# Performance work log

Measured on AMD Instinct MI355X. Metric: run time of the kernel, lower is better.

Reference implementation:

```python
import jax, jax.numpy as jnp
import numpy as np

NUM_CLASSES = 80
PRE_NMS_K = 400    # pre_nms_points / max_output_size_per_class
MAX_BOXES = 200    # max_total_size
NMS_THRESH = 0.6
SCORE_THRESH = 0.0  # iou_thresh in YoloLayer, used as score threshold/mask
SCALE_XY = (1.2, 1.1, 1.05)  # levels 3,4,5
STRIDES = (8.0, 16.0, 32.0)  # 2**level


def setup_inputs() -> dict:
    key = jax.random.key(0)
    k3, k4, k5 = jax.random.split(key, 3)
    B, C5 = 8, 3 * (NUM_CLASSES + 5)
    p3 = jax.random.normal(k3, (B, 64, 64, C5), dtype=jnp.float32)
    p4 = jax.random.normal(k4, (B, 32, 32, C5), dtype=jnp.float32)
    p5 = jax.random.normal(k5, (B, 16, 16, C5), dtype=jnp.float32)
    a3 = jnp.array([[12., 16.], [19., 36.], [40., 28.]], jnp.float32)
    a4 = jnp.array([[36., 75.], [76., 55.], [72., 146.]], jnp.float32)
    a5 = jnp.array([[142., 110.], [192., 243.], [459., 401.]], jnp.float32)
    return {"p3": p3, "p4": p4, "p5": p5, "a3": a3, "a4": a4, "a5": a5}


def _decode_level(p, anchors, stride, scale_xy):
    # p: [B,H,W,A*(C+5)] raw head output; 'original' box decode (sigmoid xy, exp wh)
    B, H, W, _ = p.shape
    A = anchors.shape[0]
    d = p.reshape(B, H, W, A, NUM_CLASSES + 5)
    txy, twh, tobj, tcls = d[..., :2], d[..., 2:4], d[..., 4:5], d[..., 5:]
    gx, gy = jnp.meshgrid(jnp.arange(W, dtype=p.dtype), jnp.arange(H, dtype=p.dtype))
    grid = jnp.stack([gx, gy], -1)[None, :, :, None, :]          # [1,H,W,1,2] (x,y)
    sxy = jnp.asarray(scale_xy, p.dtype)
    xy = (jax.nn.sigmoid(txy) * sxy - 0.5 * (sxy - 1.0) + grid) / jnp.array([W, H], p.dtype)
    wh = jnp.exp(twh) * anchors[None, None, None] / jnp.array([W * stride, H * stride], p.dtype)
    x1y1 = xy - 0.5 * wh
    x2y2 = xy + 0.5 * wh
    boxes = jnp.stack([x1y1[..., 1], x1y1[..., 0], x2y2[..., 1], x2y2[..., 0]], -1)  # yxyx
    obj = jax.nn.sigmoid(tobj)
    cls = jax.nn.sigmoid(tcls) * obj
    N = H * W * A
    return boxes.reshape(B, N, 4), cls.reshape(B, N, NUM_CLASSES), obj.reshape(B, N)


def _pairwise_iou(b):
    # b: [K,4] yxyx in [0,1]
    area = (b[:, 2] - b[:, 0]) * (b[:, 3] - b[:, 1])
    tl = jnp.maximum(b[:, None, :2], b[None, :, :2])
    br = jnp.minimum(b[:, None, 2:], b[None, :, 2:])
    wh = jnp.maximum(br - tl, 0.0)
    inter = wh[..., 0] * wh[..., 1]
    union = area[:, None] + area[None, :] - inter
    return inter / jnp.maximum(union, 1e-9)


def _greedy_nms_scores(boxes, scores):
    # boxes/scores already sorted by score descending; returns scores with suppressed -> 0
    K = scores.shape[0]
    overlap = _pairwise_iou(boxes) > NMS_THRESH
    idx = jnp.arange(K)

    def body(i, keep):
        sup = overlap[i] & (idx > i) & keep[i]
        return keep & ~sup

    keep = jax.lax.fori_loop(0, K, body, jnp.ones((K,), bool))
    return jnp.where(keep & (scores > SCORE_THRESH), scores, 0.0)


def _detections_per_image(boxes, cls_scores):
    # boxes [N,4], cls_scores [N,C] -> combined per-class NMS, top MAX_BOXES overall
    boxes = jnp.clip(boxes, 0.0, 1.0)  # combined NMS clips boxes by default

    def per_class(scores_c):
        vals, idx = jax.lax.top_k(scores_c, PRE_NMS_K)
        b = boxes[idx]
        return _greedy_nms_scores(b, vals), b

    kept_scores, kept_boxes = jax.vmap(per_class)(cls_scores.T)  # [C,K], [C,K,4]
    flat_s = kept_scores.reshape(-1)
    flat_b = kept_boxes.reshape(-1, 4)
    cls_ids = jnp.repeat(jnp.arange(NUM_CLASSES), PRE_NMS_K)
    top_s, top_i = jax.lax.top_k(flat_s, MAX_BOXES)
    top_b = flat_b[top_i]
    top_c = cls_ids[top_i].astype(jnp.float32)
    valid = top_s > 0.0
    top_b = jnp.where(valid[:, None], top_b, 0.0)
    top_c = jnp.where(valid, top_c, 0.0)
    num = jnp.sum(valid.astype(jnp.int32))
    return top_b, top_s, top_c, num


def _forward(p3, p4, p5, a3, a4, a5):
    boxes, cls_scores, obj_scores = [], [], []
    for (p, a), stride, sxy in zip(((p3, a3), (p4, a4), (p5, a5)), STRIDES, SCALE_XY):
        b, c, o = _decode_level(p, a, stride, sxy)
        boxes.append(b); cls_scores.append(c); obj_scores.append(o)
    boxes = jnp.concatenate(boxes, 1)            # [B,N,4]
    cls_scores = jnp.concatenate(cls_scores, 1)  # [B,N,C]
    obj_scores = jnp.concatenate(obj_scores, 1)  # [B,N]
    obj_mask = (obj_scores > SCORE_THRESH).astype(boxes.dtype)
    cls_mask = (cls_scores > SCORE_THRESH).astype(boxes.dtype)
    cls_scores = cls_scores * obj_mask[..., None] * cls_mask
    return jax.vmap(_detections_per_image)(boxes, cls_scores)


def reference(p3, p4, p5, a3, a4, a5):
    bbox, confidence, classes, num_detections = _forward(p3, p4, p5, a3, a4, a5)
    return bbox, confidence, classes, num_detections
```

## Files before the change

kernel.cpp:

```cpp
#include <hip/hip_runtime.h>
#include <math.h>

#define NCLS 80
#define PRE_K 400
#define MAX_BOXES 200
#define KEEP_CAP 200
#define N_TOT 16128
#define M_FIN (NCLS * KEEP_CAP)
#define NMS_T 0.6f
#define NTHR 512
#define CAP 512

typedef unsigned long long u64;
typedef unsigned int u32;

__device__ __forceinline__ float sigf(float x) { return 1.0f / (1.0f + expf(-x)); }

__device__ __forceinline__ void hist_agg(u32* hist, u32 d, bool valid, int lane)
{
    u64 act = __ballot(valid);
    while (act) {
        int ldr = __ffsll((unsigned long long)act) - 1;
        u32 dl = __shfl(d, ldr, 64);
        u64 m = __ballot(valid && d == dl);
        if (lane == ldr) atomicAdd(&hist[dl], (u32)__popcll(m));
        act &= ~m;
    }
}

__device__ __forceinline__ void digit_select(const u32* hist, int need,
                                             u32* sh_dg, u32* sh_S1, u32* sh_T, int tid)
{
    if (tid < 64) {
        const int lane = tid;
        u32 h0 = hist[4 * lane + 0], h1 = hist[4 * lane + 1];
        u32 h2 = hist[4 * lane + 2], h3 = hist[4 * lane + 3];
        u32 loc = h0 + h1 + h2 + h3;
        u32 s = loc;
#pragma unroll
        for (int off = 1; off < 64; off <<= 1) {
            u32 t = __shfl_down(s, off, 64);
            if (lane + off < 64) s += t;
        }
        u32 after = s - loc;
        u32 S3 = h3 + after, S2 = h2 + S3, S1v = h1 + S2, S0 = h0 + S1v;
        u32 Sarr[5] = { S0, S1v, S2, S3, after };
#pragma unroll
        for (int k = 0; k < 4; ++k) {
            if ((int)Sarr[k] >= need && need > (int)Sarr[k + 1]) {
                *sh_dg = (u32)(4 * lane + k);
                *sh_S1 = Sarr[k + 1];
                *sh_T  = Sarr[k] - Sarr[k + 1];
            }
        }
    }
    __syncthreads();
}

__device__ __forceinline__ void radix_topk_sort(
    const u32* __restrict__ keys, int n, int K,
    u64* cand, u32* hist, u32* scr,
    u32* sh_dg, u32* sh_S1, u32* sh_T, int* sh_gcnt, int tid)
{
    int need = K;
    digit_select(hist, need, sh_dg, sh_S1, sh_T, tid);
    u32 thr = *sh_dg; need -= (int)*sh_S1;
    int C = (K - need) + (int)*sh_T;
    int eshift = 24;

    const uint4* k4 = (const uint4*)keys;
    const int n4 = n >> 2;
    const int nIter = (n4 + NTHR - 1) / NTHR;

    for (int shift = 16; shift >= 0 && C > CAP; shift -= 8) {
        if (tid < 256) hist[tid] = 0u;
        __syncthreads();
        for (int it = 0; it < nIter; ++it) {
            int i4 = tid + it * NTHR;
            if (i4 < n4) {
                uint4 kk = k4[i4];
                if ((kk.x >> (shift + 8)) == thr) atomicAdd(&hist[(kk.x >> shift) & 255u], 1u);
                if ((kk.y >> (shift + 8)) == thr) atomicAdd(&hist[(kk.y >> shift) & 255u], 1u);
                if ((kk.z >> (shift + 8)) == thr) atomicAdd(&hist[(kk.z >> shift) & 255u], 1u);
                if ((kk.w >> (shift + 8)) == thr) atomicAdd(&hist[(kk.w >> shift) & 255u], 1u);
            }
        }
        __syncthreads();
        digit_select(hist, need, sh_dg, sh_S1, sh_T, tid);
        thr = (thr << 8) | *sh_dg; need -= (int)*sh_S1;
        C = (K - need) + (int)*sh_T;
        eshift = shift;
    }

    if (C <= CAP) {
        for (int it = 0; it < nIter; ++it) {
            int i4 = tid + it * NTHR;
            if (i4 < n4) {
                uint4 kk = k4[i4];
                int i0 = i4 << 2;
                if ((kk.x >> eshift) >= thr) { int p = atomicAdd(sh_gcnt, 1); cand[p] = ((u64)kk.x << 32) | (u32)(0xFFFFFFFFu - (u32)(i0 + 0)); }
                if ((kk.y >> eshift) >= thr) { int p = atomicAdd(sh_gcnt, 1); cand[p] = ((u64)kk.y << 32) | (u32)(0xFFFFFFFFu - (u32)(i0 + 1)); }
                if ((kk.z >> eshift) >= thr) { int p = atomicAdd(sh_gcnt, 1); cand[p] = ((u64)kk.z << 32) | (u32)(0xFFFFFFFFu - (u32)(i0 + 2)); }
                if ((kk.w >> eshift) >= thr) { int p = atomicAdd(sh_gcnt, 1); cand[p] = ((u64)kk.w << 32) | (u32)(0xFFFFFFFFu - (u32)(i0 + 3)); }
            }
        }
        __syncthreads();
        for (int t = C + tid; t < CAP; t += NTHR) cand[t] = 0ull;
    } else {
        for (int i = tid; i < n; i += NTHR) {
            u32 k = keys[i];
            if (k > thr) {
                int p = atomicAdd(sh_gcnt, 1);
                cand[p] = ((u64)k << 32) | (u32)(0xFFFFFFFFu - (u32)i);
            }
        }
        __syncthreads();
        const int G = *sh_gcnt;
        int lo = tid * 32; if (lo > n) lo = n;
        int hi = lo + 32;  if (hi > n) hi = n;
        int lc = 0;
        for (int i = lo; i < hi; ++i) if (keys[i] == thr) ++lc;
        u32* sc_cur = scr; u32* sc_oth = scr + 512;
        sc_cur[tid] = (u32)lc;
        __syncthreads();
        for (int off = 1; off < NTHR; off <<= 1) {
            sc_oth[tid] = sc_cur[tid] + ((tid >= off) ? sc_cur[tid - off] : 0u);
            __syncthreads();
            u32* tmp = sc_cur; sc_cur = sc_oth; sc_oth = tmp;
        }
        int r = (int)sc_cur[tid] - lc;
        for (int i = lo; i < hi; ++i) {
            if (keys[i] == thr) {
                if (r < need) cand[G + r] = ((u64)thr << 32) | (u32)(0xFFFFFFFFu - (u32)i);
                ++r;
            }
        }
        __syncthreads();
        for (int t = K + tid; t < CAP; t += NTHR) cand[t] = 0ull;
    }
    __syncthreads();

    u64 v = cand[tid];
#pragma unroll
    for (int k2 = 2; k2 <= 64; k2 <<= 1) {
#pragma unroll
        for (int j = k2 >> 1; j > 0; j >>= 1) {
            u64 p = __shfl_xor(v, j, 64);
            bool takeMax = ((tid & k2) == 0) ^ ((tid & j) != 0);
            v = takeMax ? (v >= p ? v : p) : (v <= p ? v : p);
        }
    }
    for (int k2 = 128; k2 <= CAP; k2 <<= 1) {
        for (int j = k2 >> 1; j >= 64; j >>= 1) {
            __syncthreads();
            cand[tid] = v;
            __syncthreads();
            u64 p = cand[tid ^ j];
            bool takeMax = ((tid & k2) == 0) ^ ((tid & j) != 0);
            v = takeMax ? (v >= p ? v : p) : (v <= p ? v : p);
        }
#pragma unroll
        for (int j = 32; j > 0; j >>= 1) {
            u64 p = __shfl_xor(v, j, 64);
            bool takeMax = ((tid & k2) == 0) ^ ((tid & j) != 0);
            v = takeMax ? (v >= p ? v : p) : (v <= p ? v : p);
        }
    }
    __syncthreads();
    cand[tid] = v;
    __syncthreads();
}

__global__ __launch_bounds__(256) void decode_kernel(
    const float* __restrict__ p3, const float* __restrict__ p4, const float* __restrict__ p5,
    const float* __restrict__ a3, const float* __restrict__ a4, const float* __restrict__ a5,
    float* __restrict__ scores, float* __restrict__ boxes)
{
    const int blk = blockIdx.x;
    const int b = blk & 7;
    const int n = ((blk >> 3) << 8) + threadIdx.x;

    const float* base; const float* anc; int logw, nn; float sx;
    if (n < 12288)      { base = p3; anc = a3; logw = 6; nn = n;         sx = 1.2f;  }
    else if (n < 15360) { base = p4; anc = a4; logw = 5; nn = n - 12288; sx = 1.1f;  }
    else                { base = p5; anc = a5; logw = 4; nn = n - 15360; sx = 1.05f; }
    const int W = 1 << logw;
    const int a = nn % 3; const int hw = nn / 3;
    const int w = hw & (W - 1); const int h = hw >> logw;
    const float winv = 1.0f / (float)W;
    const float* rec = base + ((size_t)((b * W + h) * W + w) * 255 + a * 85);

    float tx = rec[0], ty = rec[1], tw = rec[2], th = rec[3], to = rec[4];
    float sobj = sigf(to);
    float cx = (sigf(tx) * sx - 0.5f * (sx - 1.0f) + (float)w) * winv;
    float cy = (sigf(ty) * sx - 0.5f * (sx - 1.0f) + (float)h) * winv;
    float bw = expf(tw) * anc[a * 2 + 0] * (1.0f / 512.0f);
    float bh = expf(th) * anc[a * 2 + 1] * (1.0f / 512.0f);
    float x1 = cx - 0.5f * bw, x2 = cx + 0.5f * bw;
    float y1 = cy - 0.5f * bh, y2 = cy + 0.5f * bh;
    y1 = fminf(fmaxf(y1, 0.f), 1.f); x1 = fminf(fmaxf(x1, 0.f), 1.f);
    y2 = fminf(fmaxf(y2, 0.f), 1.f); x2 = fminf(fmaxf(x2, 0.f), 1.f);
    float4 bb; bb.x = y1; bb.y = x1; bb.z = y2; bb.w = x2;
    ((float4*)boxes)[b * N_TOT + n] = bb;

    float* sb = scores + (long)b * NCLS * N_TOT + n;
#pragma unroll 8
    for (int cc = 0; cc < NCLS; ++cc)
        sb[(long)cc * N_TOT] = sigf(rec[5 + cc]) * sobj;
}

__global__ __launch_bounds__(NTHR, 8) void topk_nms_fused(
    const float* __restrict__ scores, const float* __restrict__ boxes,
    float* __restrict__ ksc, float* __restrict__ kbox)
{
    __shared__ alignas(16) u64 cand[CAP];
    __shared__ u32 hist[260];
    __shared__ u32 sh_dg, sh_S1, sh_T;
    __shared__ int sh_gcnt;
    __shared__ alignas(16) u64 sup[PRE_K * 7];
    __shared__ float by1[448], bx1[448], by2[448], bx2[448], bar[448];
    __shared__ u64 keepw[7];
    __shared__ int wpre[8];
    __shared__ int sh_ncnt;

    const int tid = threadIdx.x;
    const int wv = tid >> 6;
    const int lane = tid & 63;
    const int b = blockIdx.x & 7;
    const int c = blockIdx.x >> 3;

    const u32* keys = (const u32*)(scores + (long)(b * NCLS + c) * N_TOT);

    if (tid < 260) hist[tid] = 0u;
    if (tid == 0) sh_gcnt = 0;
    __syncthreads();
    const uint4* k4 = (const uint4*)keys;
#pragma unroll
    for (int it = 0; it < 8; ++it) {
        int i4 = tid + it * NTHR;
        bool v = i4 < (N_TOT >> 2);
        u32 d0 = 0, d1 = 0, d2 = 0, d3 = 0;
        if (v) {
            uint4 kk = k4[i4];
            d0 = kk.x >> 24; d1 = kk.y >> 24; d2 = kk.z >> 24; d3 = kk.w >> 24;
        }
        hist_agg(hist, d0, v, lane);
        hist_agg(hist, d1, v, lane);
        hist_agg(hist, d2, v, lane);
        hist_agg(hist, d3, v, lane);
    }
    __syncthreads();

    radix_topk_sort(keys, N_TOT, PRE_K, cand, hist, (u32*)sup,
                    &sh_dg, &sh_S1, &sh_T, &sh_gcnt, tid);

    for (int t = tid; t < PRE_K * 7; t += NTHR) sup[t] = 0ull;

    const float4* btab = (const float4*)boxes;
    for (int t = tid; t < 448; t += NTHR) {
        float y1 = 0.f, x1 = 0.f, y2 = 0.f, x2 = 0.f;
        if (t < PRE_K) {
            u64 key = cand[t];
            if ((key >> 32) != 0ull) {
                int idx = (int)(0xFFFFFFFFu - (u32)(key & 0xFFFFFFFFull));
                float4 bb = btab[b * N_TOT + idx];
                y1 = bb.x; x1 = bb.y; y2 = bb.z; x2 = bb.w;
            }
        }
        by1[t] = y1; bx1[t] = x1; by2[t] = y2; bx2[t] = x2;
        bar[t] = (y2 - y1) * (x2 - x1);
    }
    __syncthreads();

    for (int row = wv; row < PRE_K; row += 8) {
        float ry1 = by1[row], rx1 = bx1[row], ry2 = by2[row], rx2 = bx2[row], ra = bar[row];
        int c0 = (row + 1) >> 6;
        for (int cw = c0; cw < 7; ++cw) {
            int j = (cw << 6) + lane;
            bool o = false;
            if (j > row && j < PRE_K) {
                float ty = fmaxf(ry1, by1[j]);
                float tx = fmaxf(rx1, bx1[j]);
                float by = fminf(ry2, by2[j]);
                float rx = fminf(rx2, bx2[j]);
                float hh = fmaxf(by - ty, 0.f);
                float ww = fmaxf(rx - tx, 0.f);
                float inter = hh * ww;
                float uni = ra + bar[j] - inter;
                o = (inter / fmaxf(uni, 1e-9f)) > NMS_T;
            }
            u64 m = __ballot(o);
            if (lane == 0) sup[row * 7 + cw] = m;
        }
    }
    __syncthreads();

    if (tid < 64) {
        u64 kw = (tid < 6) ? ~0ull : ((tid == 6) ? 0xFFFFull : 0ull);
        u64 s_cur = (tid < 7) ? sup[tid] : 0ull;
        for (int i = 0; i < PRE_K; ++i) {
            u64 s_next = (tid < 7 && (i + 1) < PRE_K) ? sup[(i + 1) * 7 + tid] : 0ull;
            u64 kwv = __shfl(kw, i >> 6);
            if ((kwv >> (i & 63)) & 1ull) kw &= ~s_cur;
            s_cur = s_next;
        }
        if (tid < 7) keepw[tid] = kw;
    }
    __syncthreads();

    if (tid == 0) {
        int acc = 0;
        for (int w = 0; w < 7; ++w) { wpre[w] = acc; acc += (int)__popcll(keepw[w]); }
        sh_ncnt = acc < KEEP_CAP ? acc : KEEP_CAP;
    }
    __syncthreads();

    const int blk_out = b * NCLS + c;
    float* osc = ksc + (long)blk_out * KEEP_CAP;
    float* obx = kbox + (long)blk_out * KEEP_CAP * 4;
    for (int t = tid; t < PRE_K; t += NTHR) {
        int w = t >> 6, bb = t & 63;
        u64 kwv = keepw[w];
        if ((kwv >> bb) & 1ull) {
            int pos = wpre[w] + (int)__popcll(kwv & ((1ull << bb) - 1ull));
            if (pos < KEEP_CAP) {
                osc[pos] = __uint_as_float((u32)(cand[t] >> 32));
                obx[pos * 4 + 0] = by1[t]; obx[pos * 4 + 1] = bx1[t];
                obx[pos * 4 + 2] = by2[t]; obx[pos * 4 + 3] = bx2[t];
            }
        }
    }
    for (int t = sh_ncnt + tid; t < KEEP_CAP; t += NTHR) {
        osc[t] = 0.0f;
        obx[t * 4 + 0] = 0.f; obx[t * 4 + 1] = 0.f;
        obx[t * 4 + 2] = 0.f; obx[t * 4 + 3] = 0.f;
    }
}

__global__ __launch_bounds__(NTHR, 4) void topk_nms_mono(
    const float* __restrict__ p3, const float* __restrict__ p4, const float* __restrict__ p5,
    const float* __restrict__ a3, const float* __restrict__ a4, const float* __restrict__ a5,
    float* __restrict__ ksc, float* __restrict__ kbox)
{
    __shared__ alignas(16) u32 skey[N_TOT];
    __shared__ alignas(16) u64 cand[CAP];
    __shared__ u32 hist[260];
    __shared__ u32 scr[1024];
    __shared__ u32 sh_dg, sh_S1, sh_T;
    __shared__ int sh_gcnt;
    __shared__ u64 keepw[7];
    __shared__ int wpre[8];
    __shared__ int sh_ncnt;

    const int tid = threadIdx.x;
    const int wv = tid >> 6;
    const int lane = tid & 63;
    const int b = blockIdx.x & 7;
    const int c = blockIdx.x >> 3;

    if (tid < 260) hist[tid] = 0u;
    if (tid == 0) sh_gcnt = 0;
    __syncthreads();
    for (int i = tid; i < N_TOT; i += NTHR) {
        const float* base; int H, W, n;
        if (i < 12288)      { base = p3; H = 64; W = 64; n = i; }
        else if (i < 15360) { base = p4; H = 32; W = 32; n = i - 12288; }
        else                { base = p5; H = 16; W = 16; n = i - 15360; }
        int a = n % 3; int hw = n / 3; int w = hw % W; int h = hw / W;
        const float* rec = base + (((b * H + h) * W + w) * 255 + a * 85);
        float s = sigf(rec[5 + c]) * sigf(rec[4]);
        u32 k = __float_as_uint(s);
        skey[i] = k;
        hist_agg(hist, k >> 24, true, lane);
    }
    __syncthreads();

    radix_topk_sort(skey, N_TOT, PRE_K, cand, hist, scr,
                    &sh_dg, &sh_S1, &sh_T, &sh_gcnt, tid);

    u64* sup  = (u64*)skey;
    float* by1 = (float*)(skey + 5600);
    float* bx1 = by1 + 448;
    float* by2 = bx1 + 448;
    float* bx2 = by2 + 448;
    float* bar = bx2 + 448;

    for (int t = tid; t < PRE_K * 7; t += NTHR) sup[t] = 0ull;

    for (int t = tid; t < 448; t += NTHR) {
        float y1 = 0.f, x1 = 0.f, y2 = 0.f, x2 = 0.f;
        if (t < PRE_K) {
            u64 key = cand[t];
            if ((key >> 32) != 0ull) {
                int idx = (int)(0xFFFFFFFFu - (u32)(key & 0xFFFFFFFFull));
                const float* base; const float* anc; int H, W, n; float sx, strd;
                if (idx < 12288)      { base = p3; anc = a3; H = 64; W = 64; n = idx;         sx = 1.2f;  strd = 8.f;  }
                else if (idx < 15360) { base = p4; anc = a4; H = 32; W = 32; n = idx - 12288; sx = 1.1f;  strd = 16.f; }
                else                  { base = p5; anc = a5; H = 16; W = 16; n = idx - 15360; sx = 1.05f; strd = 32.f; }
                int a = n % 3; int hw = n / 3; int w = hw % W; int h = hw / W;
                const float* rec = base + (((b * H + h) * W + w) * 255 + a * 85);
                float tx = rec[0], ty = rec[1], tw = rec[2], th = rec[3];
                float cx = (sigf(tx) * sx - 0.5f * (sx - 1.0f) + (float)w) / (float)W;
                float cy = (sigf(ty) * sx - 0.5f * (sx - 1.0f) + (float)h) / (float)H;
                float bw = expf(tw) * anc[a * 2 + 0] / ((float)W * strd);
                float bh = expf(th) * anc[a * 2 + 1] / ((float)H * strd);
                x1 = cx - 0.5f * bw; x2 = cx + 0.5f * bw;
                y1 = cy - 0.5f * bh; y2 = cy + 0.5f * bh;
                y1 = fminf(fmaxf(y1, 0.f), 1.f); x1 = fminf(fmaxf(x1, 0.f), 1.f);
                y2 = fminf(fmaxf(y2, 0.f), 1.f); x2 = fminf(fmaxf(x2, 0.f), 1.f);
            }
        }
        by1[t] = y1; bx1[t] = x1; by2[t] = y2; bx2[t] = x2;
        bar[t] = (y2 - y1) * (x2 - x1);
    }
    __syncthreads();

    for (int row = wv; row < PRE_K; row += 8) {
        float ry1 = by1[row], rx1 = bx1[row], ry2 = by2[row], rx2 = bx2[row], ra = bar[row];
        int c0 = (row + 1) >> 6;
        for (int cw = c0; cw < 7; ++cw) {
            int j = (cw << 6) + lane;
            bool o = false;
            if (j > row && j < PRE_K) {
                float ty = fmaxf(ry1, by1[j]);
                float tx = fmaxf(rx1, bx1[j]);
                float by = fminf(ry2, by2[j]);
                float rx = fminf(rx2, bx2[j]);
                float hh = fmaxf(by - ty, 0.f);
                float ww = fmaxf(rx - tx, 0.f);
                float inter = hh * ww;
                float uni = ra + bar[j] - inter;
                o = (inter / fmaxf(uni, 1e-9f)) > NMS_T;
            }
            u64 m = __ballot(o);
            if (lane == 0) sup[row * 7 + cw] = m;
        }
    }
    __syncthreads();

    if (tid < 64) {
        u64 kw = (tid < 6) ? ~0ull : ((tid == 6) ? 0xFFFFull : 0ull);
        u64 s_cur = (tid < 7) ? sup[tid] : 0ull;
        for (int i = 0; i < PRE_K; ++i) {
            u64 s_next = (tid < 7 && (i + 1) < PRE_K) ? sup[(i + 1) * 7 + tid] : 0ull;
            u64 kwv = __shfl(kw, i >> 6);
            if ((kwv >> (i & 63)) & 1ull) kw &= ~s_cur;
            s_cur = s_next;
        }
        if (tid < 7) keepw[tid] = kw;
    }
    __syncthreads();

    if (tid == 0) {
        int acc = 0;
        for (int w = 0; w < 7; ++w) { wpre[w] = acc; acc += (int)__popcll(keepw[w]); }
        sh_ncnt = acc < KEEP_CAP ? acc : KEEP_CAP;
    }
    __syncthreads();

    const int blk_out = b * NCLS + c;
    float* osc = ksc + (long)blk_out * KEEP_CAP;
    float* obx = kbox + (long)blk_out * KEEP_CAP * 4;
    for (int t = tid; t < PRE_K; t += NTHR) {
        int w = t >> 6, bb = t & 63;
        u64 kwv = keepw[w];
        if ((kwv >> bb) & 1ull) {
            int pos = wpre[w] + (int)__popcll(kwv & ((1ull << bb) - 1ull));
            if (pos < KEEP_CAP) {
                osc[pos] = __uint_as_float((u32)(cand[t] >> 32));
                obx[pos * 4 + 0] = by1[t]; obx[pos * 4 + 1] = bx1[t];
                obx[pos * 4 + 2] = by2[t]; obx[pos * 4 + 3] = bx2[t];
            }
        }
    }
    for (int t = sh_ncnt + tid; t < KEEP_CAP; t += NTHR) {
        osc[t] = 0.0f;
        obx[t * 4 + 0] = 0.f; obx[t * 4 + 1] = 0.f;
        obx[t * 4 + 2] = 0.f; obx[t * 4 + 3] = 0.f;
    }
}

__global__ __launch_bounds__(NTHR) void final_topk_kernel(
    const float* __restrict__ ksc, const float* __restrict__ kbox,
    float* __restrict__ out)
{
    __shared__ alignas(16) u64 cand[CAP];
    __shared__ u32 hist[260];
    __shared__ u32 scr[1024];
    __shared__ u32 sh_dg, sh_S1, sh_T;
    __shared__ int sh_gcnt;

    const int tid = threadIdx.x;
    const int lane = tid & 63;
    const int b = blockIdx.x;
    const u32* keys = (const u32*)(ksc + (long)b * M_FIN);

    if (tid < 260) hist[tid] = 0u;
    if (tid == 0) sh_gcnt = 0;
    __syncthreads();
    const uint4* k4 = (const uint4*)keys;
#pragma unroll
    for (int it = 0; it < 8; ++it) {
        int i4 = tid + it * NTHR;
        bool v = i4 < (M_FIN >> 2);
        u32 d0 = 0, d1 = 0, d2 = 0, d3 = 0;
        if (v) {
            uint4 kk = k4[i4];
            d0 = kk.x >> 24; d1 = kk.y >> 24; d2 = kk.z >> 24; d3 = kk.w >> 24;
        }
        hist_agg(hist, d0, v, lane);
        hist_agg(hist, d1, v, lane);
        hist_agg(hist, d2, v, lane);
        hist_agg(hist, d3, v, lane);
    }
    __syncthreads();

    radix_topk_sort(keys, M_FIN, MAX_BOXES, cand, hist, scr,
                    &sh_dg, &sh_S1, &sh_T, &sh_gcnt, tid);

    float* obb = out;
    float* ocf = out + 8 * MAX_BOXES * 4;
    float* ocl = ocf + 8 * MAX_BOXES;
    float* onm = ocl + 8 * MAX_BOXES;

    float s = 0.f;
    if (tid < MAX_BOXES) {
        u64 key = cand[tid];
        s = __uint_as_float((u32)(key >> 32));
        float y1 = 0.f, x1 = 0.f, y2 = 0.f, x2 = 0.f, cid = 0.f;
        if (s > 0.0f) {
            int i = (int)(0xFFFFFFFFu - (u32)(key & 0xFFFFFFFFull));
            int cc = i / KEEP_CAP, j = i % KEEP_CAP;
            const float* bb = kbox + (((long)b * NCLS + cc) * KEEP_CAP + j) * 4;
            y1 = bb[0]; x1 = bb[1]; y2 = bb[2]; x2 = bb[3];
            cid = (float)cc;
        }
        long o = (long)b * MAX_BOXES + tid;
        obb[o * 4 + 0] = y1; obb[o * 4 + 1] = x1; obb[o * 4 + 2] = y2; obb[o * 4 + 3] = x2;
        ocf[o] = s; ocl[o] = cid;
    }
    int cnt = __syncthreads_count(tid < MAX_BOXES && s > 0.0f);
    if (tid == 0) onm[b] = (float)cnt;
}

extern "C" void kernel_launch(void* const* d_in, const int* in_sizes, int n_in,
                              void* d_out, int out_size, void* d_ws, size_t ws_size,
                              hipStream_t stream) {
    const float* p3 = (const float*)d_in[0];
    const float* p4 = (const float*)d_in[1];
    const float* p5 = (const float*)d_in[2];
    const float* a3 = (const float*)d_in[3];
    const float* a4 = (const float*)d_in[4];
    const float* a5 = (const float*)d_in[5];
    float* out = (float*)d_out;

    const size_t score_bytes = (size_t)8 * NCLS * N_TOT * 4;
    const size_t boxes_bytes = (size_t)8 * N_TOT * 16;
    const size_t ksc_bytes   = (size_t)8 * NCLS * KEEP_CAP * 4;
    const size_t kbox_bytes  = (size_t)8 * NCLS * KEEP_CAP * 16;

    if (ws_size >= score_bytes + boxes_bytes + ksc_bytes + kbox_bytes) {
        float* scores = (float*)d_ws;
        float* boxes  = (float*)((char*)d_ws + score_bytes);
        float* ksc    = (float*)((char*)d_ws + score_bytes + boxes_bytes);
        float* kbox   = (float*)((char*)d_ws + score_bytes + boxes_bytes + ksc_bytes);
        decode_kernel<<<504, 256, 0, stream>>>(p3, p4, p5, a3, a4, a5, scores, boxes);
        topk_nms_fused<<<8 * NCLS, NTHR, 0, stream>>>(scores, boxes, ksc, kbox);
        final_topk_kernel<<<8, NTHR, 0, stream>>>(ksc, kbox, out);
    } else {
        float* ksc  = (float*)d_ws;
        float* kbox = ksc + 8 * NCLS * KEEP_CAP;
        topk_nms_mono<<<8 * NCLS, NTHR, 0, stream>>>(p3, p4, p5, a3, a4, a5, ksc, kbox);
        final_topk_kernel<<<8, NTHR, 0, stream>>>(ksc, kbox, out);
    }
}
```

Baseline: 195.6 us.

## Store 16-bit score prefixes and recompute exact scores only for candidates

Decode now writes only the upper 16 bits of each class score, which halves the dominant score workspace traffic. The top-k radix select runs on these 16-bit keys, and exact fp32 scores are recomputed from the raw head outputs only for candidates and tie-breaking. NMS is restructured into 64-row chunks that skip suppression rows for already-suppressed boxes, using a smaller shared buffer, and the launch-bounds occupancy hint drops from 8 to 6. The low-memory mono fallback path is removed, and the extra recompute loads are scattered gathers from the raw tensors.

```diff
diff --git a/kernel.cpp b/kernel.cpp
--- a/kernel.cpp
+++ b/kernel.cpp
@@ -13,8 +13,21 @@
 
 typedef unsigned long long u64;
 typedef unsigned int u32;
+typedef unsigned short u16;
 
 __device__ __forceinline__ float sigf(float x) { return 1.0f / (1.0f + expf(-x)); }
+
+__device__ __forceinline__ float score_f32(int idx, int b, int c,
+    const float* __restrict__ p3, const float* __restrict__ p4, const float* __restrict__ p5)
+{
+    const float* base; int W, n;
+    if (idx < 12288)      { base = p3; W = 64; n = idx; }
+    else if (idx < 15360) { base = p4; W = 32; n = idx - 12288; }
+    else                  { base = p5; W = 16; n = idx - 15360; }
+    int a = n % 3, hw = n / 3, w = hw % W, h = hw / W;
+    const float* rec = base + (((b * W + h) * W + w) * 255 + a * 85);
+    return sigf(rec[5 + c]) * sigf(rec[4]);
+}
 
 __device__ __forceinline__ void hist_agg(u32* hist, u32 d, bool valid, int lane)
 {
@@ -57,89 +70,8 @@
     __syncthreads();
 }
 
-__device__ __forceinline__ void radix_topk_sort(
-    const u32* __restrict__ keys, int n, int K,
-    u64* cand, u32* hist, u32* scr,
-    u32* sh_dg, u32* sh_S1, u32* sh_T, int* sh_gcnt, int tid)
-{
-    int need = K;
-    digit_select(hist, need, sh_dg, sh_S1, sh_T, tid);
-    u32 thr = *sh_dg; need -= (int)*sh_S1;
-    int C = (K - need) + (int)*sh_T;
-    int eshift = 24;
-
-    const uint4* k4 = (const uint4*)keys;
-    const int n4 = n >> 2;
-    const int nIter = (n4 + NTHR - 1) / NTHR;
-
-    for (int shift = 16; shift >= 0 && C > CAP; shift -= 8) {
-        if (tid < 256) hist[tid] = 0u;
-        __syncthreads();
-        for (int it = 0; it < nIter; ++it) {
-            int i4 = tid + it * NTHR;
-            if (i4 < n4) {
-                uint4 kk = k4[i4];
-                if ((kk.x >> (shift + 8)) == thr) atomicAdd(&hist[(kk.x >> shift) & 255u], 1u);
-                if ((kk.y >> (shift + 8)) == thr) atomicAdd(&hist[(kk.y >> shift) & 255u], 1u);
-                if ((kk.z >> (shift + 8)) == thr) atomicAdd(&hist[(kk.z >> shift) & 255u], 1u);
-                if ((kk.w >> (shift + 8)) == thr) atomicAdd(&hist[(kk.w >> shift) & 255u], 1u);
-            }
-        }
-        __syncthreads();
-        digit_select(hist, need, sh_dg, sh_S1, sh_T, tid);
-        thr = (thr << 8) | *sh_dg; need -= (int)*sh_S1;
-        C = (K - need) + (int)*sh_T;
-        eshift = shift;
-    }
-
-    if (C <= CAP) {
-        for (int it = 0; it < nIter; ++it) {
-            int i4 = tid + it * NTHR;
-            if (i4 < n4) {
-                uint4 kk = k4[i4];
-                int i0 = i4 << 2;
-                if ((kk.x >> eshift) >= thr) { int p = atomicAdd(sh_gcnt, 1); cand[p] = ((u64)kk.x << 32) | (u32)(0xFFFFFFFFu - (u32)(i0 + 0)); }
-                if ((kk.y >> eshift) >= thr) { int p = atomicAdd(sh_gcnt, 1); cand[p] = ((u64)kk.y << 32) | (u32)(0xFFFFFFFFu - (u32)(i0 + 1)); }
-                if ((kk.z >> eshift) >= thr) { int p = atomicAdd(sh_gcnt, 1); cand[p] = ((u64)kk.z << 32) | (u32)(0xFFFFFFFFu - (u32)(i0 + 2)); }
-                if ((kk.w >> eshift) >= thr) { int p = atomicAdd(sh_gcnt, 1); cand[p] = ((u64)kk.w << 32) | (u32)(0xFFFFFFFFu - (u32)(i0 + 3)); }
-            }
-        }
-        __syncthreads();
-        for (int t = C + tid; t < CAP; t += NTHR) cand[t] = 0ull;
-    } else {
-        for (int i = tid; i < n; i += NTHR) {
-            u32 k = keys[i];
-            if (k > thr) {
-                int p = atomicAdd(sh_gcnt, 1);
-                cand[p] = ((u64)k << 32) | (u32)(0xFFFFFFFFu - (u32)i);
-            }
-        }
-        __syncthreads();
-        const int G = *sh_gcnt;
-        int lo = tid * 32; if (lo > n) lo = n;
-        int hi = lo + 32;  if (hi > n) hi = n;
-        int lc = 0;
-        for (int i = lo; i < hi; ++i) if (keys[i] == thr) ++lc;
-        u32* sc_cur = scr; u32* sc_oth = scr + 512;
-        sc_cur[tid] = (u32)lc;
-        __syncthreads();
-        for (int off = 1; off < NTHR; off <<= 1) {
-            sc_oth[tid] = sc_cur[tid] + ((tid >= off) ? sc_cur[tid - off] : 0u);
-            __syncthreads();
-            u32* tmp = sc_cur; sc_cur = sc_oth; sc_oth = tmp;
-        }
-        int r = (int)sc_cur[tid] - lc;
-        for (int i = lo; i < hi; ++i) {
-            if (keys[i] == thr) {
-                if (r < need) cand[G + r] = ((u64)thr << 32) | (u32)(0xFFFFFFFFu - (u32)i);
-                ++r;
-            }
-        }
-        __syncthreads();
-        for (int t = K + tid; t < CAP; t += NTHR) cand[t] = 0ull;
-    }
-    __syncthreads();
-
+__device__ __forceinline__ void sort512(u64* cand, int tid)
+{
     u64 v = cand[tid];
 #pragma unroll
     for (int k2 = 2; k2 <= 64; k2 <<= 1) {
@@ -174,7 +106,7 @@
 __global__ __launch_bounds__(256) void decode_kernel(
     const float* __restrict__ p3, const float* __restrict__ p4, const float* __restrict__ p5,
     const float* __restrict__ a3, const float* __restrict__ a4, const float* __restrict__ a5,
-    float* __restrict__ scores, float* __restrict__ boxes)
+    u16* __restrict__ scores16, float* __restrict__ boxes)
 {
     const int blk = blockIdx.x;
     const int b = blk & 7;
@@ -203,25 +135,32 @@
     float4 bb; bb.x = y1; bb.y = x1; bb.z = y2; bb.w = x2;
     ((float4*)boxes)[b * N_TOT + n] = bb;
 
-    float* sb = scores + (long)b * NCLS * N_TOT + n;
+    u16* sb = scores16 + (long)b * NCLS * N_TOT + n;
 #pragma unroll 8
     for (int cc = 0; cc < NCLS; ++cc)
-        sb[(long)cc * N_TOT] = sigf(rec[5 + cc]) * sobj;
-}
-
-__global__ __launch_bounds__(NTHR, 8) void topk_nms_fused(
-    const float* __restrict__ scores, const float* __restrict__ boxes,
+        sb[(long)cc * N_TOT] = (u16)(__float_as_uint(sigf(rec[5 + cc]) * sobj) >> 16);
+}
+
+__global__ __launch_bounds__(NTHR, 6) void topk_nms_fused(
+    const u16* __restrict__ scores16, const float* __restrict__ boxes,
+    const float* __restrict__ p3, const float* __restrict__ p4, const float* __restrict__ p5,
     float* __restrict__ ksc, float* __restrict__ kbox)
 {
     __shared__ alignas(16) u64 cand[CAP];
     __shared__ u32 hist[260];
     __shared__ u32 sh_dg, sh_S1, sh_T;
     __shared__ int sh_gcnt;
-    __shared__ alignas(16) u64 sup[PRE_K * 7];
-    __shared__ float by1[448], bx1[448], by2[448], bx2[448], bar[448];
+    __shared__ alignas(16) float boxbuf[5 * 448];
+    __shared__ alignas(16) u64 supc[64 * 7];
     __shared__ u64 keepw[7];
     __shared__ int wpre[8];
     __shared__ int sh_ncnt;
+
+    float* by1 = boxbuf;
+    float* bx1 = boxbuf + 448;
+    float* by2 = boxbuf + 896;
+    float* bx2 = boxbuf + 1344;
+    float* bar = boxbuf + 1792;
 
     const int tid = threadIdx.x;
     const int wv = tid >> 6;
@@ -229,32 +168,175 @@
     const int b = blockIdx.x & 7;
     const int c = blockIdx.x >> 3;
 
-    const u32* keys = (const u32*)(scores + (long)(b * NCLS + c) * N_TOT);
+    const u16* keys16 = scores16 + (long)(b * NCLS + c) * N_TOT;
+    const uint4* k4 = (const uint4*)keys16;
+    const int N8 = N_TOT >> 3;
 
     if (tid < 260) hist[tid] = 0u;
     if (tid == 0) sh_gcnt = 0;
     __syncthreads();
-    const uint4* k4 = (const uint4*)keys;
-#pragma unroll
-    for (int it = 0; it < 8; ++it) {
+#pragma unroll
+    for (int it = 0; it < 4; ++it) {
         int i4 = tid + it * NTHR;
-        bool v = i4 < (N_TOT >> 2);
-        u32 d0 = 0, d1 = 0, d2 = 0, d3 = 0;
+        bool v = i4 < N8;
+        u32 e0 = 0, e1 = 0, e2 = 0, e3 = 0, e4 = 0, e5 = 0, e6 = 0, e7 = 0;
         if (v) {
             uint4 kk = k4[i4];
-            d0 = kk.x >> 24; d1 = kk.y >> 24; d2 = kk.z >> 24; d3 = kk.w >> 24;
-        }
-        hist_agg(hist, d0, v, lane);
-        hist_agg(hist, d1, v, lane);
-        hist_agg(hist, d2, v, lane);
-        hist_agg(hist, d3, v, lane);
-    }
-    __syncthreads();
-
-    radix_topk_sort(keys, N_TOT, PRE_K, cand, hist, (u32*)sup,
-                    &sh_dg, &sh_S1, &sh_T, &sh_gcnt, tid);
-
-    for (int t = tid; t < PRE_K * 7; t += NTHR) sup[t] = 0ull;
+            e0 = kk.x & 0xffffu; e1 = kk.x >> 16; e2 = kk.y & 0xffffu; e3 = kk.y >> 16;
+            e4 = kk.z & 0xffffu; e5 = kk.z >> 16; e6 = kk.w & 0xffffu; e7 = kk.w >> 16;
+        }
+        hist_agg(hist, e0 >> 8, v, lane); hist_agg(hist, e1 >> 8, v, lane);
+        hist_agg(hist, e2 >> 8, v, lane); hist_agg(hist, e3 >> 8, v, lane);
+        hist_agg(hist, e4 >> 8, v, lane); hist_agg(hist, e5 >> 8, v, lane);
+        hist_agg(hist, e6 >> 8, v, lane); hist_agg(hist, e7 >> 8, v, lane);
+    }
+    __syncthreads();
+
+    int need = PRE_K;
+    digit_select(hist, need, &sh_dg, &sh_S1, &sh_T, tid);
+    u32 thr = sh_dg; need -= (int)sh_S1;
+    int C = (PRE_K - need) + (int)sh_T;
+    int lvl = 1;
+
+    if (C > CAP) {
+        if (tid < 256) hist[tid] = 0u;
+        __syncthreads();
+#pragma unroll
+        for (int it = 0; it < 4; ++it) {
+            int i4 = tid + it * NTHR;
+            if (i4 < N8) {
+                uint4 kk = k4[i4];
+                u32 e[8] = { kk.x & 0xffffu, kk.x >> 16, kk.y & 0xffffu, kk.y >> 16,
+                             kk.z & 0xffffu, kk.z >> 16, kk.w & 0xffffu, kk.w >> 16 };
+#pragma unroll
+                for (int q = 0; q < 8; ++q)
+                    if ((e[q] >> 8) == thr) atomicAdd(&hist[e[q] & 255u], 1u);
+            }
+        }
+        __syncthreads();
+        digit_select(hist, need, &sh_dg, &sh_S1, &sh_T, tid);
+        thr = (thr << 8) | sh_dg; need -= (int)sh_S1;
+        C = (PRE_K - need) + (int)sh_T;
+        lvl = 2;
+    }
+
+    if (C > CAP) {
+        u32 t16 = thr;
+        if (tid < 256) hist[tid] = 0u;
+        __syncthreads();
+        for (int i = tid; i < N_TOT; i += NTHR) {
+            if (keys16[i] == (u16)t16) {
+                u32 kb = __float_as_uint(score_f32(i, b, c, p3, p4, p5));
+                atomicAdd(&hist[(kb >> 8) & 255u], 1u);
+            }
+        }
+        __syncthreads();
+        digit_select(hist, need, &sh_dg, &sh_S1, &sh_T, tid);
+        thr = (thr << 8) | sh_dg; need -= (int)sh_S1;
+        C = (PRE_K - need) + (int)sh_T;
+        lvl = 3;
+    }
+
+    if (C > CAP) {
+        u32 t16 = thr >> 8;
+        if (tid < 256) hist[tid] = 0u;
+        __syncthreads();
+        for (int i = tid; i < N_TOT; i += NTHR) {
+            if (keys16[i] == (u16)t16) {
+                u32 kb = __float_as_uint(score_f32(i, b, c, p3, p4, p5));
+                if ((kb >> 8) == thr) atomicAdd(&hist[kb & 255u], 1u);
+            }
+        }
+        __syncthreads();
+        digit_select(hist, need, &sh_dg, &sh_S1, &sh_T, tid);
+        thr = (thr << 8) | sh_dg; need -= (int)sh_S1;
+        C = (PRE_K - need) + (int)sh_T;
+        lvl = 4;
+    }
+
+    if (lvl <= 2) {
+#pragma unroll
+        for (int it = 0; it < 4; ++it) {
+            int i4 = tid + it * NTHR;
+            if (i4 < N8) {
+                uint4 kk = k4[i4];
+                int i0 = i4 << 3;
+                u32 e[8] = { kk.x & 0xffffu, kk.x >> 16, kk.y & 0xffffu, kk.y >> 16,
+                             kk.z & 0xffffu, kk.z >> 16, kk.w & 0xffffu, kk.w >> 16 };
+#pragma unroll
+                for (int q = 0; q < 8; ++q) {
+                    bool take = (lvl == 1) ? ((e[q] >> 8) >= thr) : (e[q] >= thr);
+                    if (take) {
+                        int p = atomicAdd(&sh_gcnt, 1);
+                        int i = i0 + q;
+                        u32 kb = __float_as_uint(score_f32(i, b, c, p3, p4, p5));
+                        cand[p] = ((u64)kb << 32) | (u32)(0xFFFFFFFFu - (u32)i);
+                    }
+                }
+            }
+        }
+        __syncthreads();
+        for (int t = C + tid; t < CAP; t += NTHR) cand[t] = 0ull;
+    } else if (C <= CAP) {
+        u32 t16 = (lvl == 3) ? (thr >> 8) : (thr >> 16);
+        for (int i = tid; i < N_TOT; i += NTHR) {
+            u32 k = keys16[i];
+            bool take = false;
+            u32 kb = 0;
+            if (k > t16) { take = true; kb = __float_as_uint(score_f32(i, b, c, p3, p4, p5)); }
+            else if (k == t16) {
+                kb = __float_as_uint(score_f32(i, b, c, p3, p4, p5));
+                take = (lvl == 3) ? ((kb >> 8) >= thr) : (kb >= thr);
+            }
+            if (take) {
+                int p = atomicAdd(&sh_gcnt, 1);
+                cand[p] = ((u64)kb << 32) | (u32)(0xFFFFFFFFu - (u32)i);
+            }
+        }
+        __syncthreads();
+        for (int t = C + tid; t < CAP; t += NTHR) cand[t] = 0ull;
+    } else {
+        u32 t16 = thr >> 16;
+        for (int i = tid; i < N_TOT; i += NTHR) {
+            u32 k = keys16[i];
+            if (k < t16) continue;
+            u32 kb = __float_as_uint(score_f32(i, b, c, p3, p4, p5));
+            if (kb > thr) {
+                int p = atomicAdd(&sh_gcnt, 1);
+                cand[p] = ((u64)kb << 32) | (u32)(0xFFFFFFFFu - (u32)i);
+            }
+        }
+        __syncthreads();
+        const int G = sh_gcnt;
+        u32* scr = (u32*)boxbuf;
+        int lo = tid * 32; if (lo > N_TOT) lo = N_TOT;
+        int hi = lo + 32;  if (hi > N_TOT) hi = N_TOT;
+        int lc = 0;
+        for (int i = lo; i < hi; ++i)
+            if (keys16[i] == (u16)t16 &&
+                __float_as_uint(score_f32(i, b, c, p3, p4, p5)) == thr) ++lc;
+        u32* sc_cur = scr; u32* sc_oth = scr + 512;
+        sc_cur[tid] = (u32)lc;
+        __syncthreads();
+        for (int off = 1; off < NTHR; off <<= 1) {
+            sc_oth[tid] = sc_cur[tid] + ((tid >= off) ? sc_cur[tid - off] : 0u);
+            __syncthreads();
+            u32* tmp = sc_cur; sc_cur = sc_oth; sc_oth = tmp;
+        }
+        int r = (int)sc_cur[tid] - lc;
+        for (int i = lo; i < hi; ++i) {
+            if (keys16[i] == (u16)t16 &&
+                __float_as_uint(score_f32(i, b, c, p3, p4, p5)) == thr) {
+                if (r < need) cand[G + r] = ((u64)thr << 32) | (u32)(0xFFFFFFFFu - (u32)i);
+                ++r;
+            }
+        }
+        __syncthreads();
+        for (int t = PRE_K + tid; t < CAP; t += NTHR) cand[t] = 0ull;
+    }
+    __syncthreads();
+
+    sort512(cand, tid);
 
     const float4* btab = (const float4*)boxes;
     for (int t = tid; t < 448; t += NTHR) {
@@ -270,43 +352,49 @@
         by1[t] = y1; bx1[t] = x1; by2[t] = y2; bx2[t] = x2;
         bar[t] = (y2 - y1) * (x2 - x1);
     }
-    __syncthreads();
-
-    for (int row = wv; row < PRE_K; row += 8) {
-        float ry1 = by1[row], rx1 = bx1[row], ry2 = by2[row], rx2 = bx2[row], ra = bar[row];
-        int c0 = (row + 1) >> 6;
-        for (int cw = c0; cw < 7; ++cw) {
-            int j = (cw << 6) + lane;
-            bool o = false;
-            if (j > row && j < PRE_K) {
-                float ty = fmaxf(ry1, by1[j]);
-                float tx = fmaxf(rx1, bx1[j]);
-                float by = fminf(ry2, by2[j]);
-                float rx = fminf(rx2, bx2[j]);
-                float hh = fmaxf(by - ty, 0.f);
-                float ww = fmaxf(rx - tx, 0.f);
-                float inter = hh * ww;
-                float uni = ra + bar[j] - inter;
-                o = (inter / fmaxf(uni, 1e-9f)) > NMS_T;
-            }
-            u64 m = __ballot(o);
-            if (lane == 0) sup[row * 7 + cw] = m;
-        }
-    }
-    __syncthreads();
-
-    if (tid < 64) {
-        u64 kw = (tid < 6) ? ~0ull : ((tid == 6) ? 0xFFFFull : 0ull);
-        u64 s_cur = (tid < 7) ? sup[tid] : 0ull;
-        for (int i = 0; i < PRE_K; ++i) {
-            u64 s_next = (tid < 7 && (i + 1) < PRE_K) ? sup[(i + 1) * 7 + tid] : 0ull;
-            u64 kwv = __shfl(kw, i >> 6);
-            if ((kwv >> (i & 63)) & 1ull) kw &= ~s_cur;
-            s_cur = s_next;
-        }
-        if (tid < 7) keepw[tid] = kw;
-    }
-    __syncthreads();
+    if (tid < 7) keepw[tid] = (tid < 6) ? ~0ull : 0xFFFFull;
+    __syncthreads();
+
+    for (int ch = 0; ch < 7; ++ch) {
+        const int rbase = ch << 6;
+        const int nrows = (PRE_K - rbase < 64) ? (PRE_K - rbase) : 64;
+        for (int r = wv; r < nrows; r += 8) {
+            int row = rbase + r;
+            if ((keepw[ch] >> r) & 1ull) {
+                float ry1 = by1[row], rx1 = bx1[row], ry2 = by2[row], rx2 = bx2[row], ra = bar[row];
+                for (int cw = ch; cw < 7; ++cw) {
+                    int j = (cw << 6) + lane;
+                    bool o = false;
+                    if (j > row && j < PRE_K) {
+                        float ty = fmaxf(ry1, by1[j]);
+                        float tx = fmaxf(rx1, bx1[j]);
+                        float by = fminf(ry2, by2[j]);
+                        float rx = fminf(rx2, bx2[j]);
+                        float hh = fmaxf(by - ty, 0.f);
+                        float ww = fmaxf(rx - tx, 0.f);
+                        float inter = hh * ww;
+                        float uni = ra + bar[j] - inter;
+                        o = (inter / fmaxf(uni, 1e-9f)) > NMS_T;
+                    }
+                    u64 m = __ballot(o);
+                    if (lane == 0) supc[r * 7 + cw] = m;
+                }
+            }
+        }
+        __syncthreads();
+        if (tid < 64) {
+            u64 kw = (tid < 7) ? keepw[tid] : 0ull;
+            u64 s_cur = (tid < 7) ? supc[tid] : 0ull;
+            for (int r = 0; r < nrows; ++r) {
+                u64 s_next = (tid < 7 && (r + 1) < nrows) ? supc[(r + 1) * 7 + tid] : 0ull;
+                u64 kwv = __shfl(kw, ch);
+                if (((kwv >> r) & 1ull) && tid >= ch) kw &= ~s_cur;
+                s_cur = s_next;
+            }
+            if (tid < 7) keepw[tid] = kw;
+        }
+        __syncthreads();
+    }
 
     if (tid == 0) {
         int acc = 0;
@@ -337,147 +425,89 @@
     }
 }
 
-__global__ __launch_bounds__(NTHR, 4) void topk_nms_mono(
-    const float* __restrict__ p3, const float* __restrict__ p4, const float* __restrict__ p5,
-    const float* __restrict__ a3, const float* __restrict__ a4, const float* __restrict__ a5,
-    float* __restrict__ ksc, float* __restrict__ kbox)
-{
-    __shared__ alignas(16) u32 skey[N_TOT];
-    __shared__ alignas(16) u64 cand[CAP];
-    __shared__ u32 hist[260];
-    __shared__ u32 scr[1024];
-    __shared__ u32 sh_dg, sh_S1, sh_T;
-    __shared__ int sh_gcnt;
-    __shared__ u64 keepw[7];
-    __shared__ int wpre[8];
-    __shared__ int sh_ncnt;
-
-    const int tid = threadIdx.x;
-    const int wv = tid >> 6;
-    const int lane = tid & 63;
-    const int b = blockIdx.x & 7;
-    const int c = blockIdx.x >> 3;
-
-    if (tid < 260) hist[tid] = 0u;
-    if (tid == 0) sh_gcnt = 0;
-    __syncthreads();
-    for (int i = tid; i < N_TOT; i += NTHR) {
-        const float* base; int H, W, n;
-        if (i < 12288)      { base = p3; H = 64; W = 64; n = i; }
-        else if (i < 15360) { base = p4; H = 32; W = 32; n = i - 12288; }
-        else                { base = p5; H = 16; W = 16; n = i - 15360; }
-        int a = n % 3; int hw = n / 3; int w = hw % W; int h = hw / W;
-        const float* rec = base + (((b * H + h) * W + w) * 255 + a * 85);
-        float s = sigf(rec[5 + c]) * sigf(rec[4]);
-        u32 k = __float_as_uint(s);
-        skey[i] = k;
-        hist_agg(hist, k >> 24, true, lane);
-    }
-    __syncthreads();
-
-    radix_topk_sort(skey, N_TOT, PRE_K, cand, hist, scr,
-                    &sh_dg, &sh_S1, &sh_T, &sh_gcnt, tid);
-
-    u64* sup  = (u64*)skey;
-    float* by1 = (float*)(skey + 5600);
-    float* bx1 = by1 + 448;
-    float* by2 = bx1 + 448;
-    float* bx2 = by2 + 448;
-    float* bar = bx2 + 448;
-
-    for (int t = tid; t < PRE_K * 7; t += NTHR) sup[t] = 0ull;
-
-    for (int t = tid; t < 448; t += NTHR) {
-        float y1 = 0.f, x1 = 0.f, y2 = 0.f, x2 = 0.f;
-        if (t < PRE_K) {
-            u64 key = cand[t];
-            if ((key >> 32) != 0ull) {
-                int idx = (int)(0xFFFFFFFFu - (u32)(key & 0xFFFFFFFFull));
-                const float* base; const float* anc; int H, W, n; float sx, strd;
-                if (idx < 12288)      { base = p3; anc = a3; H = 64; W = 64; n = idx;         sx = 1.2f;  strd = 8.f;  }
-                else if (idx < 15360) { base = p4; anc = a4; H = 32; W = 32; n = idx - 12288; sx = 1.1f;  strd = 16.f; }
-                else                  { base = p5; anc = a5; H = 16; W = 16; n = idx - 15360; sx = 1.05f; strd = 32.f; }
-                int a = n % 3; int hw = n / 3; int w = hw % W; int h = hw / W;
-                const float* rec = base + (((b * H + h) * W + w) * 255 + a * 85);
-                float tx = rec[0], ty = rec[1], tw = rec[2], th = rec[3];
-                float cx = (sigf(tx) * sx - 0.5f * (sx - 1.0f) + (float)w) / (float)W;
-                float cy = (sigf(ty) * sx - 0.5f * (sx - 1.0f) + (float)h) / (float)H;
-                float bw = expf(tw) * anc[a * 2 + 0] / ((float)W * strd);
-                float bh = expf(th) * anc[a * 2 + 1] / ((float)H * strd);
-                x1 = cx - 0.5f * bw; x2 = cx + 0.5f * bw;
-                y1 = cy - 0.5f * bh; y2 = cy + 0.5f * bh;
-                y1 = fminf(fmaxf(y1, 0.f), 1.f); x1 = fminf(fmaxf(x1, 0.f), 1.f);
-                y2 = fminf(fmaxf(y2, 0.f), 1.f); x2 = fminf(fmaxf(x2, 0.f), 1.f);
-            }
-        }
-        by1[t] = y1; bx1[t] = x1; by2[t] = y2; bx2[t] = x2;
-        bar[t] = (y2 - y1) * (x2 - x1);
-    }
-    __syncthreads();
-
-    for (int row = wv; row < PRE_K; row += 8) {
-        float ry1 = by1[row], rx1 = bx1[row], ry2 = by2[row], rx2 = bx2[row], ra = bar[row];
-        int c0 = (row + 1) >> 6;
-        for (int cw = c0; cw < 7; ++cw) {
-            int j = (cw << 6) + lane;
-            bool o = false;
-            if (j > row && j < PRE_K) {
-                float ty = fmaxf(ry1, by1[j]);
-                float tx = fmaxf(rx1, bx1[j]);
-                float by = fminf(ry2, by2[j]);
-                float rx = fminf(rx2, bx2[j]);
-                float hh = fmaxf(by - ty, 0.f);
-                float ww = fmaxf(rx - tx, 0.f);
-                float inter = hh * ww;
-                float uni = ra + bar[j] - inter;
-                o = (inter / fmaxf(uni, 1e-9f)) > NMS_T;
-            }
-            u64 m = __ballot(o);
-            if (lane == 0) sup[row * 7 + cw] = m;
-        }
-    }
-    __syncthreads();
-
-    if (tid < 64) {
-        u64 kw = (tid < 6) ? ~0ull : ((tid == 6) ? 0xFFFFull : 0ull);
-        u64 s_cur = (tid < 7) ? sup[tid] : 0ull;
-        for (int i = 0; i < PRE_K; ++i) {
-            u64 s_next = (tid < 7 && (i + 1) < PRE_K) ? sup[(i + 1) * 7 + tid] : 0ull;
-            u64 kwv = __shfl(kw, i >> 6);
-            if ((kwv >> (i & 63)) & 1ull) kw &= ~s_cur;
-            s_cur = s_next;
-        }
-        if (tid < 7) keepw[tid] = kw;
-    }
-    __syncthreads();
-
-    if (tid == 0) {
-        int acc = 0;
-        for (int w = 0; w < 7; ++w) { wpre[w] = acc; acc += (int)__popcll(keepw[w]); }
-        sh_ncnt = acc < KEEP_CAP ? acc : KEEP_CAP;
-    }
-    __syncthreads();
-
-    const int blk_out = b * NCLS + c;
-    float* osc = ksc + (long)blk_out * KEEP_CAP;
-    float* obx = kbox + (long)blk_out * KEEP_CAP * 4;
-    for (int t = tid; t < PRE_K; t += NTHR) {
-        int w = t >> 6, bb = t & 63;
-        u64 kwv = keepw[w];
-        if ((kwv >> bb) & 1ull) {
-            int pos = wpre[w] + (int)__popcll(kwv & ((1ull << bb) - 1ull));
-            if (pos < KEEP_CAP) {
-                osc[pos] = __uint_as_float((u32)(cand[t] >> 32));
-                obx[pos * 4 + 0] = by1[t]; obx[pos * 4 + 1] = bx1[t];
-                obx[pos * 4 + 2] = by2[t]; obx[pos * 4 + 3] = bx2[t];
-            }
-        }
-    }
-    for (int t = sh_ncnt + tid; t < KEEP_CAP; t += NTHR) {
-        osc[t] = 0.0f;
-        obx[t * 4 + 0] = 0.f; obx[t * 4 + 1] = 0.f;
-        obx[t * 4 + 2] = 0.f; obx[t * 4 + 3] = 0.f;
-    }
+__device__ __forceinline__ void radix_topk_sort_f32(
+    const u32* __restrict__ keys, int n, int K,
+    u64* cand, u32* hist, u32* scr,
+    u32* sh_dg, u32* sh_S1, u32* sh_T, int* sh_gcnt, int tid)
+{
+    int need = K;
+    digit_select(hist, need, sh_dg, sh_S1, sh_T, tid);
+    u32 thr = *sh_dg; need -= (int)*sh_S1;
+    int C = (K - need) + (int)*sh_T;
+    int eshift = 24;
+
+    const uint4* k4 = (const uint4*)keys;
+    const int n4 = n >> 2;
+    const int nIter = (n4 + NTHR - 1) / NTHR;
+
+    for (int shift = 16; shift >= 0 && C > CAP; shift -= 8) {
+        if (tid < 256) hist[tid] = 0u;
+        __syncthreads();
+        for (int it = 0; it < nIter; ++it) {
+            int i4 = tid + it * NTHR;
+            if (i4 < n4) {
+                uint4 kk = k4[i4];
+                if ((kk.x >> (shift + 8)) == thr) atomicAdd(&hist[(kk.x >> shift) & 255u], 1u);
+                if ((kk.y >> (shift + 8)) == thr) atomicAdd(&hist[(kk.y >> shift) & 255u], 1u);
+                if ((kk.z >> (shift + 8)) == thr) atomicAdd(&hist[(kk.z >> shift) & 255u], 1u);
+                if ((kk.w >> (shift + 8)) == thr) atomicAdd(&hist[(kk.w >> shift) & 255u], 1u);
+            }
+        }
+        __syncthreads();
+        digit_select(hist, need, sh_dg, sh_S1, sh_T, tid);
+        thr = (thr << 8) | *sh_dg; need -= (int)*sh_S1;
+        C = (K - need) + (int)*sh_T;
+        eshift = shift;
+    }
+
+    if (C <= CAP) {
+        for (int it = 0; it < nIter; ++it) {
+            int i4 = tid + it * NTHR;
+            if (i4 < n4) {
+                uint4 kk = k4[i4];
+                int i0 = i4 << 2;
+                if ((kk.x >> eshift) >= thr) { int p = atomicAdd(sh_gcnt, 1); cand[p] = ((u64)kk.x << 32) | (u32)(0xFFFFFFFFu - (u32)(i0 + 0)); }
+                if ((kk.y >> eshift) >= thr) { int p = atomicAdd(sh_gcnt, 1); cand[p] = ((u64)kk.y << 32) | (u32)(0xFFFFFFFFu - (u32)(i0 + 1)); }
+                if ((kk.z >> eshift) >= thr) { int p = atomicAdd(sh_gcnt, 1); cand[p] = ((u64)kk.z << 32) | (u32)(0xFFFFFFFFu - (u32)(i0 + 2)); }
+                if ((kk.w >> eshift) >= thr) { int p = atomicAdd(sh_gcnt, 1); cand[p] = ((u64)kk.w << 32) | (u32)(0xFFFFFFFFu - (u32)(i0 + 3)); }
+            }
+        }
+        __syncthreads();
+        for (int t = C + tid; t < CAP; t += NTHR) cand[t] = 0ull;
+    } else {
+        for (int i = tid; i < n; i += NTHR) {
+            u32 k = keys[i];
+            if (k > thr) {
+                int p = atomicAdd(sh_gcnt, 1);
+                cand[p] = ((u64)k << 32) | (u32)(0xFFFFFFFFu - (u32)i);
+            }
+        }
+        __syncthreads();
+        const int G = *sh_gcnt;
+        int lo = tid * 32; if (lo > n) lo = n;
+        int hi = lo + 32;  if (hi > n) hi = n;
+        int lc = 0;
+        for (int i = lo; i < hi; ++i) if (keys[i] == thr) ++lc;
+        u32* sc_cur = scr; u32* sc_oth = scr + 512;
+        sc_cur[tid] = (u32)lc;
+        __syncthreads();
+        for (int off = 1; off < NTHR; off <<= 1) {
+            sc_oth[tid] = sc_cur[tid] + ((tid >= off) ? sc_cur[tid - off] : 0u);
+            __syncthreads();
+            u32* tmp = sc_cur; sc_cur = sc_oth; sc_oth = tmp;
+        }
+        int r = (int)sc_cur[tid] - lc;
+        for (int i = lo; i < hi; ++i) {
+            if (keys[i] == thr) {
+                if (r < need) cand[G + r] = ((u64)thr << 32) | (u32)(0xFFFFFFFFu - (u32)i);
+                ++r;
+            }
+        }
+        __syncthreads();
+        for (int t = K + tid; t < CAP; t += NTHR) cand[t] = 0ull;
+    }
+    __syncthreads();
+    sort512(cand, tid);
 }
 
 __global__ __launch_bounds__(NTHR) void final_topk_kernel(
@@ -515,8 +545,8 @@
     }
     __syncthreads();
 
-    radix_topk_sort(keys, M_FIN, MAX_BOXES, cand, hist, scr,
-                    &sh_dg, &sh_S1, &sh_T, &sh_gcnt, tid);
+    radix_topk_sort_f32(keys, M_FIN, MAX_BOXES, cand, hist, scr,
+                        &sh_dg, &sh_S1, &sh_T, &sh_gcnt, tid);
 
     float* obb = out;
     float* ocf = out + 8 * MAX_BOXES * 4;
@@ -554,23 +584,16 @@
     const float* a5 = (const float*)d_in[5];
     float* out = (float*)d_out;
 
-    const size_t score_bytes = (size_t)8 * NCLS * N_TOT * 4;
-    const size_t boxes_bytes = (size_t)8 * N_TOT * 16;
-    const size_t ksc_bytes   = (size_t)8 * NCLS * KEEP_CAP * 4;
-    const size_t kbox_bytes  = (size_t)8 * NCLS * KEEP_CAP * 16;
-
-    if (ws_size >= score_bytes + boxes_bytes + ksc_bytes + kbox_bytes) {
-        float* scores = (float*)d_ws;
-        float* boxes  = (float*)((char*)d_ws + score_bytes);
-        float* ksc    = (float*)((char*)d_ws + score_bytes + boxes_bytes);
-        float* kbox   = (float*)((char*)d_ws + score_bytes + boxes_bytes + ksc_bytes);
-        decode_kernel<<<504, 256, 0, stream>>>(p3, p4, p5, a3, a4, a5, scores, boxes);
-        topk_nms_fused<<<8 * NCLS, NTHR, 0, stream>>>(scores, boxes, ksc, kbox);
-        final_topk_kernel<<<8, NTHR, 0, stream>>>(ksc, kbox, out);
-    } else {
-        float* ksc  = (float*)d_ws;
-        float* kbox = ksc + 8 * NCLS * KEEP_CAP;
-        topk_nms_mono<<<8 * NCLS, NTHR, 0, stream>>>(p3, p4, p5, a3, a4, a5, ksc, kbox);
-        final_topk_kernel<<<8, NTHR, 0, stream>>>(ksc, kbox, out);
-    }
-}
+    const size_t s16_bytes  = (size_t)8 * NCLS * N_TOT * 2;
+    const size_t box_bytes  = (size_t)8 * N_TOT * 16;
+    const size_t ksc_bytes  = (size_t)8 * NCLS * KEEP_CAP * 4;
+
+    u16*   scores16 = (u16*)d_ws;
+    float* boxes    = (float*)((char*)d_ws + s16_bytes);
+    float* ksc      = (float*)((char*)d_ws + s16_bytes + box_bytes);
+    float* kbox     = (float*)((char*)d_ws + s16_bytes + box_bytes + ksc_bytes);
+
+    decode_kernel<<<504, 256, 0, stream>>>(p3, p4, p5, a3, a4, a5, scores16, boxes);
+    topk_nms_fused<<<8 * NCLS, NTHR, 0, stream>>>(scores16, boxes, p3, p4, p5, ksc, kbox);
+    final_topk_kernel<<<8, NTHR, 0, stream>>>(ksc, kbox, out);
+}
```

Result: slower. 203.9 us (+4.2%).
